# Kernel optimization log

Hardware: AMD Instinct MI355X
Metric: run time of the kernel (lower is better)

Reference implementation:

```python
import jax, jax.numpy as jnp
import numpy as np

NUM_USERS = 100000
NUM_ITEMS = 50000
EMB = 64
N_SOC = 1000000
N_RAT = 1000000
BATCH = 16384
EPS = 1e-8


def setup_inputs() -> dict:
    key = jax.random.key(0)
    ks = jax.random.split(key, 8)
    user_emb = 0.01 * jax.random.normal(ks[0], (NUM_USERS, EMB), jnp.float32)
    item_emb = 0.01 * jax.random.normal(ks[1], (NUM_ITEMS, EMB), jnp.float32)
    users = jax.random.randint(ks[2], (BATCH,), 0, NUM_USERS)
    items = jax.random.randint(ks[3], (BATCH,), 0, NUM_ITEMS)
    social_src = jax.random.randint(ks[4], (N_SOC,), 0, NUM_USERS)
    social_dst = jax.random.randint(ks[5], (N_SOC,), 0, NUM_USERS)
    like_u = jax.random.randint(ks[6], (N_RAT,), 0, NUM_USERS)
    like_i = jax.random.randint(ks[7], (N_RAT,), 0, NUM_ITEMS)
    return {"user_emb": user_emb, "item_emb": item_emb, "users": users,
            "items": items, "social_src": social_src, "social_dst": social_dst,
            "like_u": like_u, "like_i": like_i}


def _deg(idx, num):
    # node degree as float column vector [num, 1]
    return jax.ops.segment_sum(jnp.ones((idx.shape[0],), jnp.float32), idx,
                               num_segments=num)[:, None]


def _seg_mean(msg, idx, num):
    s = jax.ops.segment_sum(msg, idx, num_segments=num)
    cnt = _deg(idx, num)
    return s / jnp.maximum(cnt, 1.0)


def reference(user_emb, item_emb, users, items, social_src, social_dst, like_u, like_i):
    # degree-based self-weights (deg=0 -> 1, deg>0 -> ~0)
    user_deg = _deg(like_u, NUM_USERS)            # out-degree on 'like'
    u_sw = 1.0 - user_deg / (user_deg + EPS)
    item_deg = _deg(like_i, NUM_ITEMS)            # out-degree on 'rev_like'
    i_sw = 1.0 - item_deg / (item_deg + EPS)

    def social_conv(hu):
        # mean aggregation over user->user social edges
        return _seg_mean(hu[social_src], social_dst, NUM_USERS)

    def rating_conv(hu, hi):
        # user <- mean of liked-item embeddings, plus degree-gated self
        new_u = u_sw * hu + _seg_mean(hi[like_i], like_u, NUM_USERS)
        new_i = i_sw * hi + _seg_mean(hu[like_u], like_i, NUM_ITEMS)
        return new_u, new_i

    # layer 1
    soc1 = social_conv(user_emb)
    rat_u1, rat_i1 = rating_conv(user_emb, item_emb)
    u1 = 0.5 * soc1 + 0.5 * rat_u1
    # layer 2 (stacked on per-branch states, as in the torch code)
    soc2 = social_conv(soc1)
    rat_u2, _ = rating_conv(rat_u1, rat_i1)
    u2 = 0.5 * soc2 + 0.5 * rat_u2

    # l_user = [0, 1, 2]
    final_user = user_emb + u1 + u2
    final_item = item_emb

    latest_user = final_user[users]
    latest_item = final_item[items]
    predict = jax.nn.sigmoid(jnp.sum(latest_user * latest_item, axis=1))
    return predict, latest_user, latest_item
```

## Files before the change

kernel.cpp:

```cpp
#include <hip/hip_runtime.h>
#include <hip/hip_bf16.h>

#define NUSERS 100000
#define NITEMS 50000
#define NEDGE  1000000
#define NBATCH 16384
#define CAP_LU 320000
#define EPB    2048
#define NBLK_E ((NEDGE + EPB - 1) / EPB)
#define NBW    3125
#define GGRID  2048

#define OFF_GC     0
#define OFF_GB     768
#define OFF_GCUR   1536
#define OFF_BITS   2304
#define OFF_NEED   (OFF_BITS + 3136)
#define OFF_ZEND   (OFF_NEED + NUSERS / 4)
#define OFF_IDEG   OFF_ZEND
#define OFF_UDEG   (OFF_IDEG + NITEMS)
#define OFF_SDEG   (OFF_UDEG + NUSERS)
#define OFF_ISTART (OFF_SDEG + NUSERS)
#define OFF_USTART (OFF_ISTART + NITEMS)
#define OFF_SSTART (OFF_USTART + NUSERS)
#define OFF_PARTLI (OFF_SSTART + NUSERS)
#define OFF_PARTLU (OFF_PARTLI + NEDGE)
#define OFF_PARTSD (OFF_PARTLU + CAP_LU)
#define OFF_UEMBH  OFF_PARTLI
#define OFF_CSRLI  (OFF_UEMBH + NUSERS * 32)
#define OFF_CSRLU  (OFF_CSRLI + NEDGE)
#define OFF_RI1    (OFF_CSRLU + CAP_LU)
#define OFF_SOC1   OFF_CSRLI
#define OFF_CSRSD  (OFF_SOC1 + NUSERS * 32)
#define OFF_RU1C   (OFF_CSRSD + NEDGE)
#define OFF_RU2C   (OFF_RU1C + NBATCH * 32)
#define WS_FLOATS  (OFF_RU2C + NBATCH * 32)

typedef unsigned short u16;

__device__ __forceinline__ float bf2f(u16 h) {
    union { unsigned u; float f; } c; c.u = ((unsigned)h) << 16; return c.f;
}
__device__ __forceinline__ u16 f2bf(float f) {
    union { float f; unsigned u; } c; c.f = f;
    unsigned r = c.u + 0x7fffu + ((c.u >> 16) & 1u);
    return (u16)(r >> 16);
}
__device__ __forceinline__ void acc2(unsigned w, float& a0, float& a1) {
    a0 += bf2f((u16)(w & 0xffff));
    a1 += bf2f((u16)(w >> 16));
}
__device__ __forceinline__ void acc8(uint4 w, float* a) {
    acc2(w.x, a[0], a[1]); acc2(w.y, a[2], a[3]);
    acc2(w.z, a[4], a[5]); acc2(w.w, a[6], a[7]);
}

__global__ void k_slot(const int* __restrict__ users, unsigned* __restrict__ bits,
                       unsigned char* __restrict__ needed) {
    int b = blockIdx.x * blockDim.x + threadIdx.x;
    if (b < NBATCH) {
        int u = users[b];
        atomicOr(&bits[u >> 5], 1u << (u & 31));
        needed[u] = 1;
    }
}

__global__ void k_passA(const int* __restrict__ lu, const int* __restrict__ li,
                        const int* __restrict__ sd, const int* __restrict__ ss,
                        const unsigned* __restrict__ bits, int* __restrict__ gcnt,
                        unsigned char* __restrict__ needed) {
    __shared__ int lc[768];
    __shared__ unsigned sbits[NBW];
    int t = threadIdx.x;
    for (int k = t; k < 768; k += 256) lc[k] = 0;
    for (int k = t; k < NBW; k += 256) sbits[k] = bits[k];
    __syncthreads();
    int base = blockIdx.x * EPB;
    int end = base + EPB; if (end > NEDGE) end = NEDGE;
    for (int e = base + t; e < end; e += 256) {
        int item = li[e], a = lu[e], d = sd[e];
        atomicAdd(&lc[item >> 9], 1);
        if ((sbits[a >> 5] >> (a & 31)) & 1)
            atomicAdd(&lc[256 + (a >> 9)], 1);
        atomicAdd(&lc[512 + (d >> 9)], 1);
        if ((sbits[d >> 5] >> (d & 31)) & 1)
            needed[ss[e]] = 1;
    }
    __syncthreads();
    for (int k = t; k < 768; k += 256)
        if (lc[k]) atomicAdd(&gcnt[k], lc[k]);
}

__global__ void k_passB(const int* __restrict__ gcnt, int* __restrict__ gbase,
                        int* __restrict__ gcur) {
    __shared__ int s[256];
    int t = threadIdx.x;
    for (int j = 0; j < 3; ++j) {
        int v = gcnt[j * 256 + t];
        s[t] = v;
        __syncthreads();
        for (int o = 1; o < 256; o <<= 1) {
            int x = (t >= o) ? s[t - o] : 0;
            __syncthreads();
            s[t] += x;
            __syncthreads();
        }
        int ex = s[t] - v;
        gbase[j * 256 + t] = ex;
        gcur[j * 256 + t] = ex;
        __syncthreads();
    }
}

__global__ void k_passC(const int* __restrict__ lu, const int* __restrict__ li,
                        const int* __restrict__ sd, const int* __restrict__ ss,
                        const unsigned* __restrict__ bits, int* __restrict__ gcur,
                        int* __restrict__ partLI, int* __restrict__ partLU,
                        int* __restrict__ partSD) {
    __shared__ int lc[768];
    __shared__ int go[768];
    __shared__ unsigned sbits[NBW];
    int t = threadIdx.x;
    for (int k = t; k < 768; k += 256) lc[k] = 0;
    for (int k = t; k < NBW; k += 256) sbits[k] = bits[k];
    __syncthreads();
    int base = blockIdx.x * EPB;
    int end = base + EPB; if (end > NEDGE) end = NEDGE;
    unsigned mask = 0;
    int i = 0;
    for (int e = base + t; e < end; e += 256, ++i) {
        int item = li[e], a = lu[e], d = sd[e];
        atomicAdd(&lc[item >> 9], 1);
        if ((sbits[a >> 5] >> (a & 31)) & 1) {
            atomicAdd(&lc[256 + (a >> 9)], 1);
            mask |= (1u << i);
        }
        atomicAdd(&lc[512 + (d >> 9)], 1);
    }
    __syncthreads();
    for (int k = t; k < 768; k += 256) {
        go[k] = lc[k] ? atomicAdd(&gcur[k], lc[k]) : 0;
        lc[k] = 0;
    }
    __syncthreads();
    i = 0;
    for (int e = base + t; e < end; e += 256, ++i) {
        int item = li[e], a = lu[e], d = sd[e], s_ = ss[e];
        int b0 = item >> 9;
        int r0 = atomicAdd(&lc[b0], 1);
        partLI[go[b0] + r0] = (a << 9) | (item & 511);
        if (mask & (1u << i)) {
            int b1 = 256 + (a >> 9);
            int r1 = atomicAdd(&lc[b1], 1);
            partLU[go[b1] + r1] = (item << 9) | (a & 511);
        }
        int b2 = 512 + (d >> 9);
        int r2 = atomicAdd(&lc[b2], 1);
        partSD[go[b2] + r2] = (s_ << 9) | (d & 511);
    }
}

__global__ void k_passD(const int* __restrict__ gcnt, const int* __restrict__ gbase,
                        const int* __restrict__ partLI, const int* __restrict__ partLU,
                        const int* __restrict__ partSD, int* __restrict__ csrli,
                        int* __restrict__ csrlu, int* __restrict__ csrsd,
                        int* __restrict__ ideg, int* __restrict__ udeg,
                        int* __restrict__ sdeg, int* __restrict__ istart,
                        int* __restrict__ ustart, int* __restrict__ sstart) {
    __shared__ int lcnt[512], lstart[512], sb[2][512];
    int t = threadIdx.x;
    int blk = blockIdx.x, list, b;
    const int* part; int* csr; int* deg; int* start; int n;
    if (blk < 196)      { list = 0; b = blk;       part = partLI; csr = csrli; deg = ideg; start = istart; n = NITEMS; }
    else if (blk < 392) { list = 1; b = blk - 196; part = partLU; csr = csrlu; deg = udeg; start = ustart; n = NUSERS; }
    else                { list = 2; b = blk - 392; part = partSD; csr = csrsd; deg = sdeg; start = sstart; n = NUSERS; }
    int base = gbase[list * 256 + b], cnt = gcnt[list * 256 + b];
    int node0 = b << 9;
    int M = n - node0; if (M > 512) M = 512; if (M < 0) M = 0;

    lcnt[t] = 0; lcnt[t + 256] = 0;
    __syncthreads();
    for (int i = t; i < cnt; i += 256) atomicAdd(&lcnt[part[base + i] & 511], 1);
    __syncthreads();
    sb[0][t] = lcnt[t]; sb[0][t + 256] = lcnt[t + 256];
    __syncthreads();
    int pp = 0;
    for (int o = 1; o < 512; o <<= 1) {
        int np = pp ^ 1;
        for (int k = t; k < 512; k += 256) {
            int v = sb[pp][k];
            if (k >= o) v += sb[pp][k - o];
            sb[np][k] = v;
        }
        __syncthreads();
        pp = np;
    }
    for (int k = t; k < 512; k += 256) {
        int ex = sb[pp][k] - lcnt[k];
        lstart[k] = ex;
        if (k < M) { deg[node0 + k] = lcnt[k]; start[node0 + k] = base + ex; }
    }
    __syncthreads();
    lcnt[t] = 0; lcnt[t + 256] = 0;
    __syncthreads();
    for (int i = t; i < cnt; i += 256) {
        int p = part[base + i];
        int nl = p & 511;
        int r = atomicAdd(&lcnt[nl], 1);
        csr[base + lstart[nl] + r] = p >> 9;
    }
}

__global__ void k_cvt(const float* __restrict__ src, u16* __restrict__ dst) {
    int t = blockIdx.x * 256 + threadIdx.x;
    if (t >= NUSERS * 16) return;
    float4 v = ((const float4*)src)[t];
    ushort4 o;
    o.x = f2bf(v.x); o.y = f2bf(v.y); o.z = f2bf(v.z); o.w = f2bf(v.w);
    ((ushort4*)dst)[t] = o;
}

__device__ __forceinline__ void item_store(int n, int dg, const float* __restrict__ iemb,
                                           unsigned* __restrict__ ri1, int l8,
                                           float s0, float s1, float s2, float s3,
                                           float s4, float s5, float s6, float s7) {
    float dgf = (float)dg;
    float inv = 1.0f / fmaxf(dgf, 1.0f);
    float sw  = 1.0f - dgf / (dgf + 1e-8f);
    float4 e0 = ((const float4*)(iemb + n * 64))[l8 * 2];
    float4 e1 = ((const float4*)(iemb + n * 64))[l8 * 2 + 1];
    uint4 o;
    o.x = (unsigned)f2bf(sw * e0.x + s0 * inv) | ((unsigned)f2bf(sw * e0.y + s1 * inv) << 16);
    o.y = (unsigned)f2bf(sw * e0.z + s2 * inv) | ((unsigned)f2bf(sw * e0.w + s3 * inv) << 16);
    o.z = (unsigned)f2bf(sw * e1.x + s4 * inv) | ((unsigned)f2bf(sw * e1.y + s5 * inv) << 16);
    o.w = (unsigned)f2bf(sw * e1.z + s6 * inv) | ((unsigned)f2bf(sw * e1.w + s7 * inv) << 16);
    ((uint4*)(ri1 + n * 32))[l8] = o;
}
__device__ __forceinline__ void soc_store(int n, int dg, unsigned* __restrict__ soc1, int l8,
                                          float s0, float s1, float s2, float s3,
                                          float s4, float s5, float s6, float s7) {
    float inv = 1.0f / fmaxf((float)dg, 1.0f);
    uint4 o;
    o.x = (unsigned)f2bf(s0 * inv) | ((unsigned)f2bf(s1 * inv) << 16);
    o.y = (unsigned)f2bf(s2 * inv) | ((unsigned)f2bf(s3 * inv) << 16);
    o.z = (unsigned)f2bf(s4 * inv) | ((unsigned)f2bf(s5 * inv) << 16);
    o.w = (unsigned)f2bf(s6 * inv) | ((unsigned)f2bf(s7 * inv) << 16);
    ((uint4*)(soc1 + n * 32))[l8] = o;
}

__global__ void k_gather_item(const float* __restrict__ iemb,
                              const unsigned* __restrict__ uh32,
                              const int* __restrict__ csr, const int* __restrict__ istart,
                              const int* __restrict__ ideg, unsigned* __restrict__ ri1) {
    int lane = threadIdx.x & 63;
    int wid  = blockIdx.x * 4 + (threadIdx.x >> 6);
    int nw   = gridDim.x * 4;
    int g = lane >> 3, l8 = lane & 7;
    for (int nA = wid * 2; nA < NITEMS; nA += nw * 2) {
        int nB = nA + 1;
        int jA = istart[nA], dA = ideg[nA];
        int jB = istart[nB], dB = ideg[nB];
        int cA = (lane < dA) ? csr[jA + lane] : 0;
        int cB = (lane < dB) ? csr[jB + lane] : 0;
        int kmA = dA < 64 ? dA : 64;
        int kmB = dB < 64 ? dB : 64;
        int clA = kmA > 0 ? kmA - 1 : 0;
        int clB = kmB > 0 ? kmB - 1 : 0;
        int km  = kmA > kmB ? kmA : kmB;
        float aA[8] = {0.f,0.f,0.f,0.f,0.f,0.f,0.f,0.f};
        float aB[8] = {0.f,0.f,0.f,0.f,0.f,0.f,0.f,0.f};
        for (int k = 0; k < km; k += 16) {
            int q0 = k + g, q1 = k + 8 + g;
            int iA0 = q0 < kmA ? q0 : clA;
            int iA1 = q1 < kmA ? q1 : clA;
            int iB0 = q0 < kmB ? q0 : clB;
            int iB1 = q1 < kmB ? q1 : clB;
            int rA0 = __shfl(cA, iA0), rA1 = __shfl(cA, iA1);
            int rB0 = __shfl(cB, iB0), rB1 = __shfl(cB, iB1);
            uint4 wA0 = *(const uint4*)(uh32 + rA0 * 32 + l8 * 4);
            uint4 wA1 = *(const uint4*)(uh32 + rA1 * 32 + l8 * 4);
            uint4 wB0 = *(const uint4*)(uh32 + rB0 * 32 + l8 * 4);
            uint4 wB1 = *(const uint4*)(uh32 + rB1 * 32 + l8 * 4);
            if (q0 < kmA) acc8(wA0, aA);
            if (q1 < kmA) acc8(wA1, aA);
            if (q0 < kmB) acc8(wB0, aB);
            if (q1 < kmB) acc8(wB1, aB);
        }
        for (int k = 64; k < dA; k += 8) {
            int q = k + g; int idx = q < dA ? q : dA - 1;
            int r = csr[jA + idx];
            uint4 w = *(const uint4*)(uh32 + r * 32 + l8 * 4);
            if (q < dA) acc8(w, aA);
        }
        for (int k = 64; k < dB; k += 8) {
            int q = k + g; int idx = q < dB ? q : dB - 1;
            int r = csr[jB + idx];
            uint4 w = *(const uint4*)(uh32 + r * 32 + l8 * 4);
            if (q < dB) acc8(w, aB);
        }
        #pragma unroll
        for (int off = 8; off <= 32; off <<= 1) {
            #pragma unroll
            for (int m = 0; m < 8; ++m) {
                aA[m] += __shfl_xor(aA[m], off);
                aB[m] += __shfl_xor(aB[m], off);
            }
        }
        if (g == 0)
            item_store(nA, dA, iemb, ri1, l8, aA[0],aA[1],aA[2],aA[3],aA[4],aA[5],aA[6],aA[7]);
        else if (g == 1)
            item_store(nB, dB, iemb, ri1, l8, aB[0],aB[1],aB[2],aB[3],aB[4],aB[5],aB[6],aB[7]);
    }
}

__global__ void k_batch_rat(const int* __restrict__ users, const float* __restrict__ iemb,
                            const u16* __restrict__ ri1, const int* __restrict__ csr,
                            const int* __restrict__ ustart, const int* __restrict__ udeg,
                            u16* __restrict__ ru1c, u16* __restrict__ ru2c) {
    int lane = threadIdx.x & 63;
    int wid  = blockIdx.x * 4 + (threadIdx.x >> 6);
    int nw   = gridDim.x * 4;
    for (int b = wid; b < NBATCH; b += nw) {
        int u = users[b];
        int j0 = ustart[u], dg = udeg[u];
        int cv = (lane < dg) ? csr[j0 + lane] : 0;
        int km = dg < 64 ? dg : 64;
        int cl = km > 0 ? km - 1 : 0;
        float p0=0.f,p1=0.f,p2=0.f,p3=0.f, q0=0.f,q1=0.f,q2=0.f,q3=0.f;
        for (int k = 0; k < km; k += 8) {
            int x1 = k+1 < km ? k+1 : cl, x2 = k+2 < km ? k+2 : cl;
            int x3 = k+3 < km ? k+3 : cl, x4 = k+4 < km ? k+4 : cl;
            int x5 = k+5 < km ? k+5 : cl, x6 = k+6 < km ? k+6 : cl;
            int x7 = k+7 < km ? k+7 : cl;
            int i0 = __shfl(cv, k),  i1 = __shfl(cv, x1);
            int i2 = __shfl(cv, x2), i3 = __shfl(cv, x3);
            int i4 = __shfl(cv, x4), i5 = __shfl(cv, x5);
            int i6 = __shfl(cv, x6), i7 = __shfl(cv, x7);
            float t0 = iemb[i0 * 64 + lane], t1 = iemb[i1 * 64 + lane];
            float t2 = iemb[i2 * 64 + lane], t3 = iemb[i3 * 64 + lane];
            float t4 = iemb[i4 * 64 + lane], t5 = iemb[i5 * 64 + lane];
            float t6 = iemb[i6 * 64 + lane], t7 = iemb[i7 * 64 + lane];
            float r0 = bf2f(ri1[i0 * 64 + lane]), r1 = bf2f(ri1[i1 * 64 + lane]);
            float r2 = bf2f(ri1[i2 * 64 + lane]), r3 = bf2f(ri1[i3 * 64 + lane]);
            float r4 = bf2f(ri1[i4 * 64 + lane]), r5 = bf2f(ri1[i5 * 64 + lane]);
            float r6 = bf2f(ri1[i6 * 64 + lane]), r7 = bf2f(ri1[i7 * 64 + lane]);
            p0 += t0; q0 += r0;
            if (k+1 < km) { p1 += t1; q1 += r1; }
            if (k+2 < km) { p2 += t2; q2 += r2; }
            if (k+3 < km) { p3 += t3; q3 += r3; }
            if (k+4 < km) { p0 += t4; q0 += r4; }
            if (k+5 < km) { p1 += t5; q1 += r5; }
            if (k+6 < km) { p2 += t6; q2 += r6; }
            if (k+7 < km) { p3 += t7; q3 += r7; }
        }
        for (int j = j0 + 64; j < j0 + dg; ++j) {
            int i0 = csr[j];
            p0 += iemb[i0 * 64 + lane]; q0 += bf2f(ri1[i0 * 64 + lane]);
        }
        float inv = 1.0f / fmaxf((float)dg, 1.0f);
        ru1c[b * 64 + lane] = f2bf(((p0 + p1) + (p2 + p3)) * inv);
        ru2c[b * 64 + lane] = f2bf(((q0 + q1) + (q2 + q3)) * inv);
    }
}

__global__ void k_gather_soc(const unsigned* __restrict__ uh32,
                             const int* __restrict__ csr, const int* __restrict__ sstart,
                             const int* __restrict__ sdeg,
                             const unsigned char* __restrict__ needed,
                             unsigned* __restrict__ soc1) {
    int lane = threadIdx.x & 63;
    int wid  = blockIdx.x * 4 + (threadIdx.x >> 6);
    int nw   = gridDim.x * 4;
    int g = lane >> 3, l8 = lane & 7;
    for (int nA = wid * 2; nA < NUSERS; nA += nw * 2) {
        int nB = nA + 1;
        unsigned short nd = *(const unsigned short*)(needed + nA);
        if (!nd) continue;
        int needA = nd & 0xff, needB = nd >> 8;
        int jA = sstart[nA], dA = needA ? sdeg[nA] : 0;
        int jB = sstart[nB], dB = needB ? sdeg[nB] : 0;
        int cA = (lane < dA) ? csr[jA + lane] : 0;
        int cB = (lane < dB) ? csr[jB + lane] : 0;
        int kmA = dA < 64 ? dA : 64;
        int kmB = dB < 64 ? dB : 64;
        int clA = kmA > 0 ? kmA - 1 : 0;
        int clB = kmB > 0 ? kmB - 1 : 0;
        int km  = kmA > kmB ? kmA : kmB;
        float aA[8] = {0.f,0.f,0.f,0.f,0.f,0.f,0.f,0.f};
        float aB[8] = {0.f,0.f,0.f,0.f,0.f,0.f,0.f,0.f};
        for (int k = 0; k < km; k += 16) {
            int q0 = k + g, q1 = k + 8 + g;
            int iA0 = q0 < kmA ? q0 : clA;
            int iA1 = q1 < kmA ? q1 : clA;
            int iB0 = q0 < kmB ? q0 : clB;
            int iB1 = q1 < kmB ? q1 : clB;
            int rA0 = __shfl(cA, iA0), rA1 = __shfl(cA, iA1);
            int rB0 = __shfl(cB, iB0), rB1 = __shfl(cB, iB1);
            uint4 wA0 = *(const uint4*)(uh32 + rA0 * 32 + l8 * 4);
            uint4 wA1 = *(const uint4*)(uh32 + rA1 * 32 + l8 * 4);
            uint4 wB0 = *(const uint4*)(uh32 + rB0 * 32 + l8 * 4);
            uint4 wB1 = *(const uint4*)(uh32 + rB1 * 32 + l8 * 4);
            if (q0 < kmA) acc8(wA0, aA);
            if (q1 < kmA) acc8(wA1, aA);
            if (q0 < kmB) acc8(wB0, aB);
            if (q1 < kmB) acc8(wB1, aB);
        }
        for (int k = 64; k < dA; k += 8) {
            int q = k + g; int idx = q < dA ? q : dA - 1;
            int r = csr[jA + idx];
            uint4 w = *(const uint4*)(uh32 + r * 32 + l8 * 4);
            if (q < dA) acc8(w, aA);
        }
        for (int k = 64; k < dB; k += 8) {
            int q = k + g; int idx = q < dB ? q : dB - 1;
            int r = csr[jB + idx];
            uint4 w = *(const uint4*)(uh32 + r * 32 + l8 * 4);
            if (q < dB) acc8(w, aB);
        }
        #pragma unroll
        for (int off = 8; off <= 32; off <<= 1) {
            #pragma unroll
            for (int m = 0; m < 8; ++m) {
                aA[m] += __shfl_xor(aA[m], off);
                aB[m] += __shfl_xor(aB[m], off);
            }
        }
        if (g == 0 && needA)
            soc_store(nA, dA, soc1, l8, aA[0],aA[1],aA[2],aA[3],aA[4],aA[5],aA[6],aA[7]);
        else if (g == 1 && needB)
            soc_store(nB, dB, soc1, l8, aB[0],aB[1],aB[2],aB[3],aB[4],aB[5],aB[6],aB[7]);
    }
}

__global__ void k_final(const int* __restrict__ users, const int* __restrict__ items,
                        const float* __restrict__ uemb, const float* __restrict__ iemb,
                        const u16* __restrict__ soc1, const int* __restrict__ csr,
                        const int* __restrict__ sstart, const int* __restrict__ sdeg,
                        const u16* __restrict__ ru1c, const u16* __restrict__ ru2c,
                        const int* __restrict__ udeg, float* __restrict__ out) {
    int d   = threadIdx.x & 63;
    int wid = blockIdx.x * 4 + (threadIdx.x >> 6);
    int nw  = gridDim.x * 4;
    for (int b = wid; b < NBATCH; b += nw) {
        int u = users[b], it = items[b];
        int j0 = sstart[u], dg = sdeg[u];
        int cv = (d < dg) ? csr[j0 + d] : 0;
        int km = dg < 64 ? dg : 64;
        int cl = km > 0 ? km - 1 : 0;
        float s0=0.f, s1a=0.f, s2a=0.f, s3a=0.f;
        for (int k = 0; k < km; k += 8) {
            int x1 = k+1 < km ? k+1 : cl, x2 = k+2 < km ? k+2 : cl;
            int x3 = k+3 < km ? k+3 : cl, x4 = k+4 < km ? k+4 : cl;
            int x5 = k+5 < km ? k+5 : cl, x6 = k+6 < km ? k+6 : cl;
            int x7 = k+7 < km ? k+7 : cl;
            int c0 = __shfl(cv, k),  c1 = __shfl(cv, x1);
            int c2 = __shfl(cv, x2), c3 = __shfl(cv, x3);
            int c4 = __shfl(cv, x4), c5 = __shfl(cv, x5);
            int c6 = __shfl(cv, x6), c7 = __shfl(cv, x7);
            float f0 = bf2f(soc1[c0 * 64 + d]), f1 = bf2f(soc1[c1 * 64 + d]);
            float f2 = bf2f(soc1[c2 * 64 + d]), f3 = bf2f(soc1[c3 * 64 + d]);
            float f4 = bf2f(soc1[c4 * 64 + d]), f5 = bf2f(soc1[c5 * 64 + d]);
            float f6 = bf2f(soc1[c6 * 64 + d]), f7 = bf2f(soc1[c7 * 64 + d]);
            s0 += f0;
            if (k+1 < km) s1a += f1;
            if (k+2 < km) s2a += f2;
            if (k+3 < km) s3a += f3;
            if (k+4 < km) s0  += f4;
            if (k+5 < km) s1a += f5;
            if (k+6 < km) s2a += f6;
            if (k+7 < km) s3a += f7;
        }
        for (int j = j0 + 64; j < j0 + dg; ++j)
            s0 += bf2f(soc1[csr[j] * 64 + d]);
        float s2 = ((s0 + s1a) + (s2a + s3a)) / fmaxf((float)dg, 1.0f);
        float ud = (float)udeg[u];
        float usw = 1.0f - ud / (ud + 1e-8f);
        float ue = uemb[u * 64 + d];
        float s1 = bf2f(soc1[u * 64 + d]);
        float r1 = usw * ue + bf2f(ru1c[b * 64 + d]);
        float r2 = usw * r1 + bf2f(ru2c[b * 64 + d]);
        float fu = ue + 0.5f * (s1 + r1) + 0.5f * (s2 + r2);
        float iv = iemb[it * 64 + d];
        out[NBATCH + b * 64 + d]               = fu;
        out[NBATCH + NBATCH * 64 + b * 64 + d] = iv;
        float p = fu * iv;
        #pragma unroll
        for (int o = 32; o > 0; o >>= 1) p += __shfl_down(p, o);
        if (d == 0) out[b] = 1.0f / (1.0f + __expf(-p));
    }
}

extern "C" void kernel_launch(void* const* d_in, const int* in_sizes, int n_in,
                              void* d_out, int out_size, void* d_ws, size_t ws_size,
                              hipStream_t stream) {
    const float* uemb  = (const float*)d_in[0];
    const float* iemb  = (const float*)d_in[1];
    const int*   users = (const int*)d_in[2];
    const int*   items = (const int*)d_in[3];
    const int*   ssrc  = (const int*)d_in[4];
    const int*   sdst  = (const int*)d_in[5];
    const int*   lu    = (const int*)d_in[6];
    const int*   li    = (const int*)d_in[7];
    float* out = (float*)d_out;

    if (ws_size < (size_t)WS_FLOATS * 4) return;

    int*           W      = (int*)d_ws;
    int*           gcnt   = W + OFF_GC;
    int*           gbase  = W + OFF_GB;
    int*           gcur   = W + OFF_GCUR;
    unsigned*      bits   = (unsigned*)(W + OFF_BITS);
    unsigned char* needed = (unsigned char*)(W + OFF_NEED);
    int*           ideg   = W + OFF_IDEG;
    int*           udeg   = W + OFF_UDEG;
    int*           sdeg   = W + OFF_SDEG;
    int*           istart = W + OFF_ISTART;
    int*           ustart = W + OFF_USTART;
    int*           sstart = W + OFF_SSTART;
    int*           partLI = W + OFF_PARTLI;
    int*           partLU = W + OFF_PARTLU;
    int*           partSD = W + OFF_PARTSD;
    u16*           uembh  = (u16*)(W + OFF_UEMBH);
    int*           csrli  = W + OFF_CSRLI;
    int*           csrlu  = W + OFF_CSRLU;
    int*           csrsd  = W + OFF_CSRSD;
    u16*           ri1    = (u16*)(W + OFF_RI1);
    u16*           soc1   = (u16*)(W + OFF_SOC1);
    u16*           ru1c   = (u16*)(W + OFF_RU1C);
    u16*           ru2c   = (u16*)(W + OFF_RU2C);

    hipMemsetAsync(d_ws, 0, (size_t)OFF_ZEND * 4, stream);

    const int B = 256;

    k_slot<<<(NBATCH + B - 1) / B, B, 0, stream>>>(users, bits, needed);
    k_passA<<<NBLK_E, B, 0, stream>>>(lu, li, sdst, ssrc, bits, gcnt, needed);
    k_passB<<<1, B, 0, stream>>>(gcnt, gbase, gcur);
    k_passC<<<NBLK_E, B, 0, stream>>>(lu, li, sdst, ssrc, bits, gcur,
                                      partLI, partLU, partSD);
    k_passD<<<588, B, 0, stream>>>(gcnt, gbase, partLI, partLU, partSD,
                                   csrli, csrlu, csrsd, ideg, udeg, sdeg,
                                   istart, ustart, sstart);

    k_cvt<<<(NUSERS * 16 + B - 1) / B, B, 0, stream>>>(uemb, uembh);

    k_gather_item<<<GGRID, B, 0, stream>>>(iemb, (const unsigned*)uembh,
                                           csrli, istart, ideg, (unsigned*)ri1);
    k_batch_rat<<<GGRID, B, 0, stream>>>(users, iemb, ri1, csrlu, ustart,
                                         udeg, ru1c, ru2c);
    k_gather_soc<<<GGRID, B, 0, stream>>>((const unsigned*)uembh, csrsd,
                                          sstart, sdeg, needed, (unsigned*)soc1);

    k_final<<<GGRID, B, 0, stream>>>(users, items, uemb, iemb, soc1,
                                     csrsd, sstart, sdeg, ru1c, ru2c, udeg, out);
}
```

Baseline: 274.0 us.

## Fuse item and social gathers into one kernel, merge batch rating into final

The item-side rating gather and the social gather, which both read the bf16 user table, now run as one kernel over a combined work range. The per-batch rating aggregation is folded into the final kernel, so the ru1c/ru2c intermediates disappear. This drops two launches and their serialization gaps, removes an intermediate write and read, and lets the two independent gathers share the GPU. The workspace layout is reorganized so soc1, ri1 and the CSR arrays no longer alias each other. The cost is that the final kernel does more serial work per warp.

```diff
diff --git a/kernel.cpp b/kernel.cpp
--- a/kernel.cpp
+++ b/kernel.cpp
@@ -23,18 +23,16 @@
 #define OFF_ISTART (OFF_SDEG + NUSERS)
 #define OFF_USTART (OFF_ISTART + NITEMS)
 #define OFF_SSTART (OFF_USTART + NUSERS)
-#define OFF_PARTLI (OFF_SSTART + NUSERS)
+#define OFF_PARTLI 530464
 #define OFF_PARTLU (OFF_PARTLI + NEDGE)
 #define OFF_PARTSD (OFF_PARTLU + CAP_LU)
 #define OFF_UEMBH  OFF_PARTLI
 #define OFF_CSRLI  (OFF_UEMBH + NUSERS * 32)
 #define OFF_CSRLU  (OFF_CSRLI + NEDGE)
-#define OFF_RI1    (OFF_CSRLU + CAP_LU)
-#define OFF_SOC1   OFF_CSRLI
-#define OFF_CSRSD  (OFF_SOC1 + NUSERS * 32)
-#define OFF_RU1C   (OFF_CSRSD + NEDGE)
-#define OFF_RU2C   (OFF_RU1C + NBATCH * 32)
-#define WS_FLOATS  (OFF_RU2C + NBATCH * 32)
+#define OFF_CSRSD  (OFF_CSRLU + CAP_LU)
+#define OFF_RI1    (OFF_CSRSD + NEDGE)
+#define OFF_SOC1   (OFF_RI1 + NITEMS * 32)
+#define WS_FLOATS  (OFF_SOC1 + NUSERS * 32)
 
 typedef unsigned short u16;
 
@@ -222,263 +220,208 @@
 
 __device__ __forceinline__ void item_store(int n, int dg, const float* __restrict__ iemb,
                                            unsigned* __restrict__ ri1, int l8,
-                                           float s0, float s1, float s2, float s3,
-                                           float s4, float s5, float s6, float s7) {
+                                           const float* __restrict__ s) {
     float dgf = (float)dg;
     float inv = 1.0f / fmaxf(dgf, 1.0f);
     float sw  = 1.0f - dgf / (dgf + 1e-8f);
     float4 e0 = ((const float4*)(iemb + n * 64))[l8 * 2];
     float4 e1 = ((const float4*)(iemb + n * 64))[l8 * 2 + 1];
     uint4 o;
-    o.x = (unsigned)f2bf(sw * e0.x + s0 * inv) | ((unsigned)f2bf(sw * e0.y + s1 * inv) << 16);
-    o.y = (unsigned)f2bf(sw * e0.z + s2 * inv) | ((unsigned)f2bf(sw * e0.w + s3 * inv) << 16);
-    o.z = (unsigned)f2bf(sw * e1.x + s4 * inv) | ((unsigned)f2bf(sw * e1.y + s5 * inv) << 16);
-    o.w = (unsigned)f2bf(sw * e1.z + s6 * inv) | ((unsigned)f2bf(sw * e1.w + s7 * inv) << 16);
+    o.x = (unsigned)f2bf(sw * e0.x + s[0] * inv) | ((unsigned)f2bf(sw * e0.y + s[1] * inv) << 16);
+    o.y = (unsigned)f2bf(sw * e0.z + s[2] * inv) | ((unsigned)f2bf(sw * e0.w + s[3] * inv) << 16);
+    o.z = (unsigned)f2bf(sw * e1.x + s[4] * inv) | ((unsigned)f2bf(sw * e1.y + s[5] * inv) << 16);
+    o.w = (unsigned)f2bf(sw * e1.z + s[6] * inv) | ((unsigned)f2bf(sw * e1.w + s[7] * inv) << 16);
     ((uint4*)(ri1 + n * 32))[l8] = o;
 }
 __device__ __forceinline__ void soc_store(int n, int dg, unsigned* __restrict__ soc1, int l8,
-                                          float s0, float s1, float s2, float s3,
-                                          float s4, float s5, float s6, float s7) {
+                                          const float* __restrict__ s) {
     float inv = 1.0f / fmaxf((float)dg, 1.0f);
     uint4 o;
-    o.x = (unsigned)f2bf(s0 * inv) | ((unsigned)f2bf(s1 * inv) << 16);
-    o.y = (unsigned)f2bf(s2 * inv) | ((unsigned)f2bf(s3 * inv) << 16);
-    o.z = (unsigned)f2bf(s4 * inv) | ((unsigned)f2bf(s5 * inv) << 16);
-    o.w = (unsigned)f2bf(s6 * inv) | ((unsigned)f2bf(s7 * inv) << 16);
+    o.x = (unsigned)f2bf(s[0] * inv) | ((unsigned)f2bf(s[1] * inv) << 16);
+    o.y = (unsigned)f2bf(s[2] * inv) | ((unsigned)f2bf(s[3] * inv) << 16);
+    o.z = (unsigned)f2bf(s[4] * inv) | ((unsigned)f2bf(s[5] * inv) << 16);
+    o.w = (unsigned)f2bf(s[6] * inv) | ((unsigned)f2bf(s[7] * inv) << 16);
     ((uint4*)(soc1 + n * 32))[l8] = o;
 }
 
-__global__ void k_gather_item(const float* __restrict__ iemb,
-                              const unsigned* __restrict__ uh32,
-                              const int* __restrict__ csr, const int* __restrict__ istart,
-                              const int* __restrict__ ideg, unsigned* __restrict__ ri1) {
+__device__ __forceinline__ void gather_pair(const unsigned* __restrict__ uh32,
+                                            const int* __restrict__ csr,
+                                            int jA, int dA, int jB, int dB,
+                                            int lane, int g, int l8,
+                                            float* __restrict__ aA,
+                                            float* __restrict__ aB) {
+    int cA = (lane < dA) ? csr[jA + lane] : 0;
+    int cB = (lane < dB) ? csr[jB + lane] : 0;
+    int kmA = dA < 64 ? dA : 64;
+    int kmB = dB < 64 ? dB : 64;
+    int clA = kmA > 0 ? kmA - 1 : 0;
+    int clB = kmB > 0 ? kmB - 1 : 0;
+    int km  = kmA > kmB ? kmA : kmB;
+    for (int k = 0; k < km; k += 16) {
+        int q0 = k + g, q1 = k + 8 + g;
+        int iA0 = q0 < kmA ? q0 : clA;
+        int iA1 = q1 < kmA ? q1 : clA;
+        int iB0 = q0 < kmB ? q0 : clB;
+        int iB1 = q1 < kmB ? q1 : clB;
+        int rA0 = __shfl(cA, iA0), rA1 = __shfl(cA, iA1);
+        int rB0 = __shfl(cB, iB0), rB1 = __shfl(cB, iB1);
+        uint4 wA0 = *(const uint4*)(uh32 + rA0 * 32 + l8 * 4);
+        uint4 wA1 = *(const uint4*)(uh32 + rA1 * 32 + l8 * 4);
+        uint4 wB0 = *(const uint4*)(uh32 + rB0 * 32 + l8 * 4);
+        uint4 wB1 = *(const uint4*)(uh32 + rB1 * 32 + l8 * 4);
+        if (q0 < kmA) acc8(wA0, aA);
+        if (q1 < kmA) acc8(wA1, aA);
+        if (q0 < kmB) acc8(wB0, aB);
+        if (q1 < kmB) acc8(wB1, aB);
+    }
+    for (int k = 64; k < dA; k += 8) {
+        int q = k + g; int idx = q < dA ? q : dA - 1;
+        int r = csr[jA + idx];
+        uint4 w = *(const uint4*)(uh32 + r * 32 + l8 * 4);
+        if (q < dA) acc8(w, aA);
+    }
+    for (int k = 64; k < dB; k += 8) {
+        int q = k + g; int idx = q < dB ? q : dB - 1;
+        int r = csr[jB + idx];
+        uint4 w = *(const uint4*)(uh32 + r * 32 + l8 * 4);
+        if (q < dB) acc8(w, aB);
+    }
+    #pragma unroll
+    for (int off = 8; off <= 32; off <<= 1) {
+        #pragma unroll
+        for (int m = 0; m < 8; ++m) {
+            aA[m] += __shfl_xor(aA[m], off);
+            aB[m] += __shfl_xor(aB[m], off);
+        }
+    }
+}
+
+__global__ void k_gather_fused(const float* __restrict__ iemb,
+                               const unsigned* __restrict__ uh32,
+                               const int* __restrict__ csrli, const int* __restrict__ istart,
+                               const int* __restrict__ ideg, unsigned* __restrict__ ri1,
+                               const int* __restrict__ csrsd, const int* __restrict__ sstart,
+                               const int* __restrict__ sdeg,
+                               const unsigned char* __restrict__ needed,
+                               unsigned* __restrict__ soc1) {
     int lane = threadIdx.x & 63;
     int wid  = blockIdx.x * 4 + (threadIdx.x >> 6);
     int nw   = gridDim.x * 4;
     int g = lane >> 3, l8 = lane & 7;
-    for (int nA = wid * 2; nA < NITEMS; nA += nw * 2) {
-        int nB = nA + 1;
-        int jA = istart[nA], dA = ideg[nA];
-        int jB = istart[nB], dB = ideg[nB];
-        int cA = (lane < dA) ? csr[jA + lane] : 0;
-        int cB = (lane < dB) ? csr[jB + lane] : 0;
-        int kmA = dA < 64 ? dA : 64;
-        int kmB = dB < 64 ? dB : 64;
-        int clA = kmA > 0 ? kmA - 1 : 0;
-        int clB = kmB > 0 ? kmB - 1 : 0;
-        int km  = kmA > kmB ? kmA : kmB;
-        float aA[8] = {0.f,0.f,0.f,0.f,0.f,0.f,0.f,0.f};
-        float aB[8] = {0.f,0.f,0.f,0.f,0.f,0.f,0.f,0.f};
-        for (int k = 0; k < km; k += 16) {
-            int q0 = k + g, q1 = k + 8 + g;
-            int iA0 = q0 < kmA ? q0 : clA;
-            int iA1 = q1 < kmA ? q1 : clA;
-            int iB0 = q0 < kmB ? q0 : clB;
-            int iB1 = q1 < kmB ? q1 : clB;
-            int rA0 = __shfl(cA, iA0), rA1 = __shfl(cA, iA1);
-            int rB0 = __shfl(cB, iB0), rB1 = __shfl(cB, iB1);
-            uint4 wA0 = *(const uint4*)(uh32 + rA0 * 32 + l8 * 4);
-            uint4 wA1 = *(const uint4*)(uh32 + rA1 * 32 + l8 * 4);
-            uint4 wB0 = *(const uint4*)(uh32 + rB0 * 32 + l8 * 4);
-            uint4 wB1 = *(const uint4*)(uh32 + rB1 * 32 + l8 * 4);
-            if (q0 < kmA) acc8(wA0, aA);
-            if (q1 < kmA) acc8(wA1, aA);
-            if (q0 < kmB) acc8(wB0, aB);
-            if (q1 < kmB) acc8(wB1, aB);
-        }
-        for (int k = 64; k < dA; k += 8) {
-            int q = k + g; int idx = q < dA ? q : dA - 1;
-            int r = csr[jA + idx];
-            uint4 w = *(const uint4*)(uh32 + r * 32 + l8 * 4);
-            if (q < dA) acc8(w, aA);
-        }
-        for (int k = 64; k < dB; k += 8) {
-            int q = k + g; int idx = q < dB ? q : dB - 1;
-            int r = csr[jB + idx];
-            uint4 w = *(const uint4*)(uh32 + r * 32 + l8 * 4);
-            if (q < dB) acc8(w, aB);
-        }
-        #pragma unroll
-        for (int off = 8; off <= 32; off <<= 1) {
-            #pragma unroll
-            for (int m = 0; m < 8; ++m) {
-                aA[m] += __shfl_xor(aA[m], off);
-                aB[m] += __shfl_xor(aB[m], off);
-            }
-        }
-        if (g == 0)
-            item_store(nA, dA, iemb, ri1, l8, aA[0],aA[1],aA[2],aA[3],aA[4],aA[5],aA[6],aA[7]);
-        else if (g == 1)
-            item_store(nB, dB, iemb, ri1, l8, aB[0],aB[1],aB[2],aB[3],aB[4],aB[5],aB[6],aB[7]);
-    }
-}
-
-__global__ void k_batch_rat(const int* __restrict__ users, const float* __restrict__ iemb,
-                            const u16* __restrict__ ri1, const int* __restrict__ csr,
-                            const int* __restrict__ ustart, const int* __restrict__ udeg,
-                            u16* __restrict__ ru1c, u16* __restrict__ ru2c) {
-    int lane = threadIdx.x & 63;
-    int wid  = blockIdx.x * 4 + (threadIdx.x >> 6);
-    int nw   = gridDim.x * 4;
-    for (int b = wid; b < NBATCH; b += nw) {
-        int u = users[b];
-        int j0 = ustart[u], dg = udeg[u];
-        int cv = (lane < dg) ? csr[j0 + lane] : 0;
-        int km = dg < 64 ? dg : 64;
-        int cl = km > 0 ? km - 1 : 0;
-        float p0=0.f,p1=0.f,p2=0.f,p3=0.f, q0=0.f,q1=0.f,q2=0.f,q3=0.f;
-        for (int k = 0; k < km; k += 8) {
-            int x1 = k+1 < km ? k+1 : cl, x2 = k+2 < km ? k+2 : cl;
-            int x3 = k+3 < km ? k+3 : cl, x4 = k+4 < km ? k+4 : cl;
-            int x5 = k+5 < km ? k+5 : cl, x6 = k+6 < km ? k+6 : cl;
-            int x7 = k+7 < km ? k+7 : cl;
-            int i0 = __shfl(cv, k),  i1 = __shfl(cv, x1);
-            int i2 = __shfl(cv, x2), i3 = __shfl(cv, x3);
-            int i4 = __shfl(cv, x4), i5 = __shfl(cv, x5);
-            int i6 = __shfl(cv, x6), i7 = __shfl(cv, x7);
-            float t0 = iemb[i0 * 64 + lane], t1 = iemb[i1 * 64 + lane];
-            float t2 = iemb[i2 * 64 + lane], t3 = iemb[i3 * 64 + lane];
-            float t4 = iemb[i4 * 64 + lane], t5 = iemb[i5 * 64 + lane];
-            float t6 = iemb[i6 * 64 + lane], t7 = iemb[i7 * 64 + lane];
-            float r0 = bf2f(ri1[i0 * 64 + lane]), r1 = bf2f(ri1[i1 * 64 + lane]);
-            float r2 = bf2f(ri1[i2 * 64 + lane]), r3 = bf2f(ri1[i3 * 64 + lane]);
-            float r4 = bf2f(ri1[i4 * 64 + lane]), r5 = bf2f(ri1[i5 * 64 + lane]);
-            float r6 = bf2f(ri1[i6 * 64 + lane]), r7 = bf2f(ri1[i7 * 64 + lane]);
-            p0 += t0; q0 += r0;
-            if (k+1 < km) { p1 += t1; q1 += r1; }
-            if (k+2 < km) { p2 += t2; q2 += r2; }
-            if (k+3 < km) { p3 += t3; q3 += r3; }
-            if (k+4 < km) { p0 += t4; q0 += r4; }
-            if (k+5 < km) { p1 += t5; q1 += r5; }
-            if (k+6 < km) { p2 += t6; q2 += r6; }
-            if (k+7 < km) { p3 += t7; q3 += r7; }
-        }
-        for (int j = j0 + 64; j < j0 + dg; ++j) {
-            int i0 = csr[j];
-            p0 += iemb[i0 * 64 + lane]; q0 += bf2f(ri1[i0 * 64 + lane]);
-        }
-        float inv = 1.0f / fmaxf((float)dg, 1.0f);
-        ru1c[b * 64 + lane] = f2bf(((p0 + p1) + (p2 + p3)) * inv);
-        ru2c[b * 64 + lane] = f2bf(((q0 + q1) + (q2 + q3)) * inv);
-    }
-}
-
-__global__ void k_gather_soc(const unsigned* __restrict__ uh32,
-                             const int* __restrict__ csr, const int* __restrict__ sstart,
-                             const int* __restrict__ sdeg,
-                             const unsigned char* __restrict__ needed,
-                             unsigned* __restrict__ soc1) {
-    int lane = threadIdx.x & 63;
-    int wid  = blockIdx.x * 4 + (threadIdx.x >> 6);
-    int nw   = gridDim.x * 4;
-    int g = lane >> 3, l8 = lane & 7;
-    for (int nA = wid * 2; nA < NUSERS; nA += nw * 2) {
-        int nB = nA + 1;
-        unsigned short nd = *(const unsigned short*)(needed + nA);
-        if (!nd) continue;
-        int needA = nd & 0xff, needB = nd >> 8;
-        int jA = sstart[nA], dA = needA ? sdeg[nA] : 0;
-        int jB = sstart[nB], dB = needB ? sdeg[nB] : 0;
-        int cA = (lane < dA) ? csr[jA + lane] : 0;
-        int cB = (lane < dB) ? csr[jB + lane] : 0;
-        int kmA = dA < 64 ? dA : 64;
-        int kmB = dB < 64 ? dB : 64;
-        int clA = kmA > 0 ? kmA - 1 : 0;
-        int clB = kmB > 0 ? kmB - 1 : 0;
-        int km  = kmA > kmB ? kmA : kmB;
-        float aA[8] = {0.f,0.f,0.f,0.f,0.f,0.f,0.f,0.f};
-        float aB[8] = {0.f,0.f,0.f,0.f,0.f,0.f,0.f,0.f};
-        for (int k = 0; k < km; k += 16) {
-            int q0 = k + g, q1 = k + 8 + g;
-            int iA0 = q0 < kmA ? q0 : clA;
-            int iA1 = q1 < kmA ? q1 : clA;
-            int iB0 = q0 < kmB ? q0 : clB;
-            int iB1 = q1 < kmB ? q1 : clB;
-            int rA0 = __shfl(cA, iA0), rA1 = __shfl(cA, iA1);
-            int rB0 = __shfl(cB, iB0), rB1 = __shfl(cB, iB1);
-            uint4 wA0 = *(const uint4*)(uh32 + rA0 * 32 + l8 * 4);
-            uint4 wA1 = *(const uint4*)(uh32 + rA1 * 32 + l8 * 4);
-            uint4 wB0 = *(const uint4*)(uh32 + rB0 * 32 + l8 * 4);
-            uint4 wB1 = *(const uint4*)(uh32 + rB1 * 32 + l8 * 4);
-            if (q0 < kmA) acc8(wA0, aA);
-            if (q1 < kmA) acc8(wA1, aA);
-            if (q0 < kmB) acc8(wB0, aB);
-            if (q1 < kmB) acc8(wB1, aB);
-        }
-        for (int k = 64; k < dA; k += 8) {
-            int q = k + g; int idx = q < dA ? q : dA - 1;
-            int r = csr[jA + idx];
-            uint4 w = *(const uint4*)(uh32 + r * 32 + l8 * 4);
-            if (q < dA) acc8(w, aA);
-        }
-        for (int k = 64; k < dB; k += 8) {
-            int q = k + g; int idx = q < dB ? q : dB - 1;
-            int r = csr[jB + idx];
-            uint4 w = *(const uint4*)(uh32 + r * 32 + l8 * 4);
-            if (q < dB) acc8(w, aB);
-        }
-        #pragma unroll
-        for (int off = 8; off <= 32; off <<= 1) {
-            #pragma unroll
-            for (int m = 0; m < 8; ++m) {
-                aA[m] += __shfl_xor(aA[m], off);
-                aB[m] += __shfl_xor(aB[m], off);
-            }
-        }
-        if (g == 0 && needA)
-            soc_store(nA, dA, soc1, l8, aA[0],aA[1],aA[2],aA[3],aA[4],aA[5],aA[6],aA[7]);
-        else if (g == 1 && needB)
-            soc_store(nB, dB, soc1, l8, aB[0],aB[1],aB[2],aB[3],aB[4],aB[5],aB[6],aB[7]);
-    }
-}
-
-__global__ void k_final(const int* __restrict__ users, const int* __restrict__ items,
-                        const float* __restrict__ uemb, const float* __restrict__ iemb,
-                        const u16* __restrict__ soc1, const int* __restrict__ csr,
-                        const int* __restrict__ sstart, const int* __restrict__ sdeg,
-                        const u16* __restrict__ ru1c, const u16* __restrict__ ru2c,
-                        const int* __restrict__ udeg, float* __restrict__ out) {
+    const int NPI = NITEMS / 2;
+    const int NP  = NPI + NUSERS / 2;
+    for (int w = wid; w < NP; w += nw) {
+        if (w < NPI) {
+            int nA = w * 2, nB = nA + 1;
+            int jA = istart[nA], dA = ideg[nA];
+            int jB = istart[nB], dB = ideg[nB];
+            float aA[8] = {0.f,0.f,0.f,0.f,0.f,0.f,0.f,0.f};
+            float aB[8] = {0.f,0.f,0.f,0.f,0.f,0.f,0.f,0.f};
+            gather_pair(uh32, csrli, jA, dA, jB, dB, lane, g, l8, aA, aB);
+            if (g == 0)      item_store(nA, dA, iemb, ri1, l8, aA);
+            else if (g == 1) item_store(nB, dB, iemb, ri1, l8, aB);
+        } else {
+            int nA = (w - NPI) * 2, nB = nA + 1;
+            unsigned short nd = *(const unsigned short*)(needed + nA);
+            if (!nd) continue;
+            int needA = nd & 0xff, needB = nd >> 8;
+            int jA = sstart[nA], dA = needA ? sdeg[nA] : 0;
+            int jB = sstart[nB], dB = needB ? sdeg[nB] : 0;
+            float aA[8] = {0.f,0.f,0.f,0.f,0.f,0.f,0.f,0.f};
+            float aB[8] = {0.f,0.f,0.f,0.f,0.f,0.f,0.f,0.f};
+            gather_pair(uh32, csrsd, jA, dA, jB, dB, lane, g, l8, aA, aB);
+            if (g == 0 && needA)      soc_store(nA, dA, soc1, l8, aA);
+            else if (g == 1 && needB) soc_store(nB, dB, soc1, l8, aB);
+        }
+    }
+}
+
+__global__ void k_final2(const int* __restrict__ users, const int* __restrict__ items,
+                         const float* __restrict__ uemb, const float* __restrict__ iemb,
+                         const u16* __restrict__ ri1, const int* __restrict__ csrlu,
+                         const int* __restrict__ ustart, const int* __restrict__ udeg,
+                         const u16* __restrict__ soc1, const int* __restrict__ csrsd,
+                         const int* __restrict__ sstart, const int* __restrict__ sdeg,
+                         float* __restrict__ out) {
     int d   = threadIdx.x & 63;
     int wid = blockIdx.x * 4 + (threadIdx.x >> 6);
     int nw  = gridDim.x * 4;
     for (int b = wid; b < NBATCH; b += nw) {
         int u = users[b], it = items[b];
-        int j0 = sstart[u], dg = sdeg[u];
-        int cv = (d < dg) ? csr[j0 + d] : 0;
-        int km = dg < 64 ? dg : 64;
-        int cl = km > 0 ? km - 1 : 0;
+        int ju = ustart[u], du = udeg[u];
+        int js = sstart[u], ds = sdeg[u];
+        int cvU = (d < du) ? csrlu[ju + d] : 0;
+        int cvS = (d < ds) ? csrsd[js + d] : 0;
+        int kmu = du < 64 ? du : 64;
+        int clu = kmu > 0 ? kmu - 1 : 0;
+        float p0=0.f,p1=0.f,p2=0.f,p3=0.f, q0=0.f,q1=0.f,q2=0.f,q3=0.f;
+        for (int k = 0; k < kmu; k += 8) {
+            int x1 = k+1 < kmu ? k+1 : clu, x2 = k+2 < kmu ? k+2 : clu;
+            int x3 = k+3 < kmu ? k+3 : clu, x4 = k+4 < kmu ? k+4 : clu;
+            int x5 = k+5 < kmu ? k+5 : clu, x6 = k+6 < kmu ? k+6 : clu;
+            int x7 = k+7 < kmu ? k+7 : clu;
+            int i0 = __shfl(cvU, k),  i1 = __shfl(cvU, x1);
+            int i2 = __shfl(cvU, x2), i3 = __shfl(cvU, x3);
+            int i4 = __shfl(cvU, x4), i5 = __shfl(cvU, x5);
+            int i6 = __shfl(cvU, x6), i7 = __shfl(cvU, x7);
+            float t0 = iemb[i0 * 64 + d], t1 = iemb[i1 * 64 + d];
+            float t2 = iemb[i2 * 64 + d], t3 = iemb[i3 * 64 + d];
+            float t4 = iemb[i4 * 64 + d], t5 = iemb[i5 * 64 + d];
+            float t6 = iemb[i6 * 64 + d], t7 = iemb[i7 * 64 + d];
+            float r0 = bf2f(ri1[i0 * 64 + d]), r1 = bf2f(ri1[i1 * 64 + d]);
+            float r2 = bf2f(ri1[i2 * 64 + d]), r3 = bf2f(ri1[i3 * 64 + d]);
+            float r4 = bf2f(ri1[i4 * 64 + d]), r5 = bf2f(ri1[i5 * 64 + d]);
+            float r6 = bf2f(ri1[i6 * 64 + d]), r7 = bf2f(ri1[i7 * 64 + d]);
+            p0 += t0; q0 += r0;
+            if (k+1 < kmu) { p1 += t1; q1 += r1; }
+            if (k+2 < kmu) { p2 += t2; q2 += r2; }
+            if (k+3 < kmu) { p3 += t3; q3 += r3; }
+            if (k+4 < kmu) { p0 += t4; q0 += r4; }
+            if (k+5 < kmu) { p1 += t5; q1 += r5; }
+            if (k+6 < kmu) { p2 += t6; q2 += r6; }
+            if (k+7 < kmu) { p3 += t7; q3 += r7; }
+        }
+        for (int j = ju + 64; j < ju + du; ++j) {
+            int i0 = csrlu[j];
+            p0 += iemb[i0 * 64 + d]; q0 += bf2f(ri1[i0 * 64 + d]);
+        }
+        int kms = ds < 64 ? ds : 64;
+        int cls = kms > 0 ? kms - 1 : 0;
         float s0=0.f, s1a=0.f, s2a=0.f, s3a=0.f;
-        for (int k = 0; k < km; k += 8) {
-            int x1 = k+1 < km ? k+1 : cl, x2 = k+2 < km ? k+2 : cl;
-            int x3 = k+3 < km ? k+3 : cl, x4 = k+4 < km ? k+4 : cl;
-            int x5 = k+5 < km ? k+5 : cl, x6 = k+6 < km ? k+6 : cl;
-            int x7 = k+7 < km ? k+7 : cl;
-            int c0 = __shfl(cv, k),  c1 = __shfl(cv, x1);
-            int c2 = __shfl(cv, x2), c3 = __shfl(cv, x3);
-            int c4 = __shfl(cv, x4), c5 = __shfl(cv, x5);
-            int c6 = __shfl(cv, x6), c7 = __shfl(cv, x7);
+        for (int k = 0; k < kms; k += 8) {
+            int x1 = k+1 < kms ? k+1 : cls, x2 = k+2 < kms ? k+2 : cls;
+            int x3 = k+3 < kms ? k+3 : cls, x4 = k+4 < kms ? k+4 : cls;
+            int x5 = k+5 < kms ? k+5 : cls, x6 = k+6 < kms ? k+6 : cls;
+            int x7 = k+7 < kms ? k+7 : cls;
+            int c0 = __shfl(cvS, k),  c1 = __shfl(cvS, x1);
+            int c2 = __shfl(cvS, x2), c3 = __shfl(cvS, x3);
+            int c4 = __shfl(cvS, x4), c5 = __shfl(cvS, x5);
+            int c6 = __shfl(cvS, x6), c7 = __shfl(cvS, x7);
             float f0 = bf2f(soc1[c0 * 64 + d]), f1 = bf2f(soc1[c1 * 64 + d]);
             float f2 = bf2f(soc1[c2 * 64 + d]), f3 = bf2f(soc1[c3 * 64 + d]);
             float f4 = bf2f(soc1[c4 * 64 + d]), f5 = bf2f(soc1[c5 * 64 + d]);
             float f6 = bf2f(soc1[c6 * 64 + d]), f7 = bf2f(soc1[c7 * 64 + d]);
             s0 += f0;
-            if (k+1 < km) s1a += f1;
-            if (k+2 < km) s2a += f2;
-            if (k+3 < km) s3a += f3;
-            if (k+4 < km) s0  += f4;
-            if (k+5 < km) s1a += f5;
-            if (k+6 < km) s2a += f6;
-            if (k+7 < km) s3a += f7;
-        }
-        for (int j = j0 + 64; j < j0 + dg; ++j)
-            s0 += bf2f(soc1[csr[j] * 64 + d]);
-        float s2 = ((s0 + s1a) + (s2a + s3a)) / fmaxf((float)dg, 1.0f);
-        float ud = (float)udeg[u];
+            if (k+1 < kms) s1a += f1;
+            if (k+2 < kms) s2a += f2;
+            if (k+3 < kms) s3a += f3;
+            if (k+4 < kms) s0  += f4;
+            if (k+5 < kms) s1a += f5;
+            if (k+6 < kms) s2a += f6;
+            if (k+7 < kms) s3a += f7;
+        }
+        for (int j = js + 64; j < js + ds; ++j)
+            s0 += bf2f(soc1[csrsd[j] * 64 + d]);
+        float invU = 1.0f / fmaxf((float)du, 1.0f);
+        float ru1 = ((p0 + p1) + (p2 + p3)) * invU;
+        float ru2 = ((q0 + q1) + (q2 + q3)) * invU;
+        float s2 = ((s0 + s1a) + (s2a + s3a)) / fmaxf((float)ds, 1.0f);
+        float ud = (float)du;
         float usw = 1.0f - ud / (ud + 1e-8f);
         float ue = uemb[u * 64 + d];
         float s1 = bf2f(soc1[u * 64 + d]);
-        float r1 = usw * ue + bf2f(ru1c[b * 64 + d]);
-        float r2 = usw * r1 + bf2f(ru2c[b * 64 + d]);
+        float r1 = usw * ue + ru1;
+        float r2 = usw * r1 + ru2;
         float fu = ue + 0.5f * (s1 + r1) + 0.5f * (s2 + r2);
         float iv = iemb[it * 64 + d];
         out[NBATCH + b * 64 + d]               = fu;
@@ -526,8 +469,6 @@
     int*           csrsd  = W + OFF_CSRSD;
     u16*           ri1    = (u16*)(W + OFF_RI1);
     u16*           soc1   = (u16*)(W + OFF_SOC1);
-    u16*           ru1c   = (u16*)(W + OFF_RU1C);
-    u16*           ru2c   = (u16*)(W + OFF_RU2C);
 
     hipMemsetAsync(d_ws, 0, (size_t)OFF_ZEND * 4, stream);
 
@@ -544,13 +485,11 @@
 
     k_cvt<<<(NUSERS * 16 + B - 1) / B, B, 0, stream>>>(uemb, uembh);
 
-    k_gather_item<<<GGRID, B, 0, stream>>>(iemb, (const unsigned*)uembh,
-                                           csrli, istart, ideg, (unsigned*)ri1);
-    k_batch_rat<<<GGRID, B, 0, stream>>>(users, iemb, ri1, csrlu, ustart,
-                                         udeg, ru1c, ru2c);
-    k_gather_soc<<<GGRID, B, 0, stream>>>((const unsigned*)uembh, csrsd,
-                                          sstart, sdeg, needed, (unsigned*)soc1);
-
-    k_final<<<GGRID, B, 0, stream>>>(users, items, uemb, iemb, soc1,
-                                     csrsd, sstart, sdeg, ru1c, ru2c, udeg, out);
-}
+    k_gather_fused<<<GGRID, B, 0, stream>>>(iemb, (const unsigned*)uembh,
+                                            csrli, istart, ideg, (unsigned*)ri1,
+                                            csrsd, sstart, sdeg, needed,
+                                            (unsigned*)soc1);
+
+    k_final2<<<GGRID, B, 0, stream>>>(users, items, uemb, iemb, ri1, csrlu,
+                                      ustart, udeg, soc1, csrsd, sstart, sdeg, out);
+}
```

After: 252.6 us. -7.8%, faster.
